# Kernel optimization log

Measured on AMD Instinct MI355X. Metric: run time of the kernel, lower is better.

## Reference

```python
import jax, jax.numpy as jnp
import numpy as np

H = 1536
NH = 24
HD = 64
B = 2
S = 2048


def _rotate_half(x):
    x1, x2 = x[..., : HD // 2], x[..., HD // 2 :]
    return jnp.concatenate((-x2, x1), axis=-1)


def setup_inputs() -> dict:
    key = jax.random.key(0)
    ks = jax.random.split(key, 8)
    scale = 1.0 / np.sqrt(H)
    pos = jnp.arange(S)[:, None]
    inv_freq = 1.0 / (10000.0 ** (jnp.arange(0, HD, 2, dtype=jnp.float32) / HD))
    ang = pos * inv_freq[None, :]
    ang = jnp.concatenate([ang, ang], axis=-1)  # [S, HD]
    return {
        "hidden_states": jax.random.normal(ks[0], (B, S, H), jnp.float32),
        "rope_cos": jnp.cos(ang),
        "rope_sin": jnp.sin(ang),
        "wq": jax.random.normal(ks[1], (H, H), jnp.float32) * scale,
        "bq": jnp.zeros((H,), jnp.float32),
        "wk": jax.random.normal(ks[2], (H, H), jnp.float32) * scale,
        "bk": jnp.zeros((H,), jnp.float32),
        "wv": jax.random.normal(ks[3], (H, H), jnp.float32) * scale,
        "bv": jnp.zeros((H,), jnp.float32),
        "wo": jax.random.normal(ks[4], (H, H), jnp.float32) * scale,
        "bo": jnp.zeros((H,), jnp.float32),
    }


def reference(hidden_states, rope_cos, rope_sin, wq, bq, wk, bk, wv, bv, wo, bo):
    b, s, _ = hidden_states.shape
    # QKV projections (torch Linear: x @ W.T + b)
    q = hidden_states @ wq.T + bq
    k = hidden_states @ wk.T + bk
    v = hidden_states @ wv.T + bv
    # [B, NH, S, HD]
    q = q.reshape(b, s, NH, HD).transpose(0, 2, 1, 3)
    k = k.reshape(b, s, NH, HD).transpose(0, 2, 1, 3)
    v = v.reshape(b, s, NH, HD).transpose(0, 2, 1, 3)
    # RoPE: cos/sin broadcast over batch & heads
    cos = rope_cos[None, None, :, :]
    sin = rope_sin[None, None, :, :]
    q = q * cos + _rotate_half(q) * sin
    k = k * cos + _rotate_half(k) * sin
    # SDPA
    scores = jnp.einsum("bhqd,bhkd->bhqk", q, k) / jnp.sqrt(jnp.float32(HD))
    attn = jax.nn.softmax(scores, axis=-1)
    out = jnp.einsum("bhqk,bhkd->bhqd", attn, v)
    out = out.transpose(0, 2, 1, 3).reshape(b, s, NH * HD)
    return out @ wo.T + bo
```

## Files before the change

kernel.cpp:

```cpp
#include <hip/hip_runtime.h>
#include <hip/hip_bf16.h>
#include <cstdint>

namespace {
constexpr int H_  = 1536;
constexpr int NH_ = 24;
constexpr int HD_ = 64;
constexpr int B_  = 2;
constexpr int S_  = 2048;
constexpr int M_  = B_ * S_;
constexpr int KD_ = H_;
}

typedef __attribute__((ext_vector_type(8)))  short bf16x8;
typedef __attribute__((ext_vector_type(4)))  float f32x4;
typedef __attribute__((ext_vector_type(16))) float f32x16;

__device__ __forceinline__ unsigned short f2bf_fast(float x) {
    return (unsigned short)((__float_as_uint(x) + 0x8000u) >> 16);
}
__device__ __forceinline__ unsigned pack2bf(float b_hi, float a_lo) {
    const unsigned ub = __float_as_uint(b_hi) + 0x8000u;
    const unsigned ua = __float_as_uint(a_lo) + 0x8000u;
    return (ub & 0xffff0000u) | (ua >> 16);
}

__device__ __forceinline__ void gload16(const short* g, short* l) {
    __builtin_amdgcn_global_load_lds(
        (const __attribute__((address_space(1))) unsigned int*)g,
        (__attribute__((address_space(3))) unsigned int*)l, 16, 0, 0);
}

__global__ __launch_bounds__(256)
void cast_all(const float* __restrict__ X,
              const float* __restrict__ wq, const float* __restrict__ wk,
              const float* __restrict__ wv, const float* __restrict__ wo,
              short* __restrict__ Xh,
              short* __restrict__ Wqh, short* __restrict__ Wkh,
              short* __restrict__ Wvh, short* __restrict__ Woh)
{
    constexpr int XB = (M_*H_) / 1024;
    constexpr int WB = (H_*H_) / 1024;
    const int bid = blockIdx.x;
    const float* src; short* dst; int off;
    if (bid < XB)            { src = X;  dst = Xh;  off = bid; }
    else {
        const int r = bid - XB, wsel = r / WB; off = r % WB;
        if      (wsel == 0)  { src = wq; dst = Wqh; }
        else if (wsel == 1)  { src = wk; dst = Wkh; }
        else if (wsel == 2)  { src = wv; dst = Wvh; }
        else                 { src = wo; dst = Woh; }
    }
    const int i = (off * 256 + threadIdx.x) * 4;
    const float4 v = *(const float4*)&src[i];
    uint2 o;
    o.x = pack2bf(v.y, v.x);
    o.y = pack2bf(v.w, v.z);
    *(uint2*)&dst[i] = o;
}

template<int KIND>
__global__ __launch_bounds__(256, 4)
void gemm_bf16(const short* __restrict__ A_g,
               const short* __restrict__ Wq, const short* __restrict__ Wk,
               const short* __restrict__ Wv,
               const float* __restrict__ bq, const float* __restrict__ bk,
               const float* __restrict__ bv,
               const float* __restrict__ cosb, const float* __restrict__ sinb,
               short* __restrict__ Qb, short* __restrict__ Kb,
               short* __restrict__ Vt, float* __restrict__ outf)
{
    __shared__ short Ah[128*64], Bh[128*64];

    const int t    = threadIdx.x;
    const int lane = t & 63;
    const int w    = t >> 6;
    const int wr   = w >> 1, wc = w & 1;
    const int l15  = lane & 15;
    const int grp  = lane >> 4;

    const int xcd = blockIdx.x & 7;
    const int off = blockIdx.x >> 3;
    const int m_idx = xcd * 4 + (off & 3);
    const int rest  = off >> 2;
    const int n_idx = rest % 12;
    const int zi    = (KIND == 0) ? rest / 12 : 3;

    const int m0 = m_idx * 128;
    const int n0 = n_idx * 128;

    const short* bhg; const float* bias;
    if (KIND == 0) {
        if      (zi == 0) { bhg = Wq; bias = bq; }
        else if (zi == 1) { bhg = Wk; bias = bk; }
        else              { bhg = Wv; bias = bv; }
    } else {
        bhg = Wq; bias = bq;
    }

    f32x4 acc[4][4];
#pragma unroll
    for (int i = 0; i < 4; ++i)
#pragma unroll
        for (int j = 0; j < 4; ++j) acc[i][j] = (f32x4){0.f, 0.f, 0.f, 0.f};

    const int srow  = lane >> 3;
    const int sslot = (lane & 7) ^ srow;

    for (int kt = 0; kt < KD_; kt += 64) {
        __syncthreads();
#pragma unroll
        for (int cc = 0; cc < 4; ++cc) {
            const int c = w * 4 + cc;
            const int r = c * 8 + srow;
            gload16(A_g + (size_t)(m0 + r) * KD_ + kt + sslot * 8, Ah + c * 512);
            gload16(bhg + (size_t)(n0 + r) * KD_ + kt + sslot * 8, Bh + c * 512);
        }
        __syncthreads();

#pragma unroll
        for (int kk = 0; kk < 2; ++kk) {
            bf16x8 af[4], bfr[4];
#pragma unroll
            for (int i = 0; i < 4; ++i) {
                const int ra = wr * 64 + i * 16 + l15;
                af[i]  = *(const bf16x8*)&Ah[ra * 64 + (((kk*4 + grp) ^ (ra & 7)) << 3)];
                const int rb = wc * 64 + i * 16 + l15;
                bfr[i] = *(const bf16x8*)&Bh[rb * 64 + (((kk*4 + grp) ^ (rb & 7)) << 3)];
            }
#pragma unroll
            for (int i = 0; i < 4; ++i)
#pragma unroll
                for (int j = 0; j < 4; ++j)
                    acc[i][j] = __builtin_amdgcn_mfma_f32_16x16x32_bf16(af[i], bfr[j], acc[i][j], 0, 0, 0);
        }
    }

    float bn[4];
#pragma unroll
    for (int ni = 0; ni < 4; ++ni) bn[ni] = bias[n0 + wc * 64 + ni * 16 + l15];
    const int hw = (n0 + wc * 64) >> 6;

    if (KIND == 1) {
#pragma unroll
        for (int mi = 0; mi < 4; ++mi)
#pragma unroll
            for (int r = 0; r < 4; ++r) {
                const int m = m0 + wr * 64 + mi * 16 + grp * 4 + r;
#pragma unroll
                for (int ni = 0; ni < 4; ++ni)
                    outf[(size_t)m * H_ + n0 + wc * 64 + ni * 16 + l15] =
                        acc[mi][ni][r] + bn[ni];
            }
        return;
    }

    if (zi == 2) {
        const int b = m0 >> 11;
#pragma unroll
        for (int mi = 0; mi < 4; ++mi) {
            const int sb = (m0 & (S_ - 1)) + wr * 64 + mi * 16 + grp * 4;
#pragma unroll
            for (int ni = 0; ni < 4; ++ni) {
                const int d = ni * 16 + l15;
                uint2 o;
                o.x = pack2bf(acc[mi][ni][1] + bn[ni], acc[mi][ni][0] + bn[ni]);
                o.y = pack2bf(acc[mi][ni][3] + bn[ni], acc[mi][ni][2] + bn[ni]);
                *(uint2*)&Vt[((size_t)(b * NH_ + hw) * HD_ + d) * S_ + sb] = o;
            }
        }
        return;
    }

    const float sc = (zi == 0) ? 0.18033688011112042f : 1.0f;
    short* dst = (zi == 0) ? Qb : Kb;
#pragma unroll
    for (int mi = 0; mi < 4; ++mi)
#pragma unroll
        for (int r = 0; r < 4; ++r) {
            const int m = m0 + wr * 64 + mi * 16 + grp * 4 + r;
            const int b = m >> 11;
            const int s = m & (S_ - 1);
#pragma unroll
            for (int ni = 0; ni < 4; ++ni) {
                const int d  = ni * 16 + l15;
                const float val = acc[mi][ni][r] + bn[ni];
                const float pv  = acc[mi][ni ^ 2][r] + bn[ni ^ 2];
                const float cs = cosb[s * HD_ + d];
                const float sn = sinb[s * HD_ + d];
                const float rot = (ni < 2) ? -pv : pv;
                dst[((size_t)(b * NH_ + hw) * S_ + s) * HD_ + d] =
                    (short)f2bf_fast((val * cs + rot * sn) * sc);
            }
        }
}

__global__ __launch_bounds__(256, 3)
void attn_mfma(const short* __restrict__ Q, const short* __restrict__ K,
               const short* __restrict__ Vt, short* __restrict__ AO)
{
    __shared__ short Ks[2][4096];
    __shared__ short Vs[2][4096];

    const int t    = threadIdx.x;
    const int lane = t & 63;
    const int wid  = t >> 6;
    const int bh   = blockIdx.y;
    const int q0   = blockIdx.x * 128;

    const int l31 = lane & 31;
    const int hi  = lane >> 5;
    const int sw7 = lane & 7;

    const short* Qg = Q  + ((size_t)bh * S_ + q0 + wid*32) * HD_;
    const short* Kg = K  + (size_t)bh * S_ * HD_;
    const short* Vg = Vt + (size_t)bh * HD_ * S_;

    bf16x8 qf[4];
#pragma unroll
    for (int kk = 0; kk < 4; ++kk)
        qf[kk] = *(const bf16x8*)(Qg + (size_t)l31*HD_ + kk*16 + hi*8);

    f32x16 oacc[2];
#pragma unroll
    for (int nt = 0; nt < 2; ++nt)
#pragma unroll
        for (int r = 0; r < 16; ++r) oacc[nt][r] = 0.f;
    float lacc = 0.f;

    auto stageKV = [&](int b, int kt) {
#pragma unroll
        for (int cc = 0; cc < 2; ++cc) {
            const int d   = cc * 256 + t;
            const int row = d >> 3;
            const int sg  = (d & 7) ^ (row & 7);
            gload16(Kg + (size_t)(kt + row) * HD_ + sg * 8, &Ks[b][d * 8]);
            gload16(Vg + (size_t)row * S_ + kt + sg * 8,    &Vs[b][d * 8]);
        }
    };

    stageKV(0, 0);
    __syncthreads();
    int cur = 0;

    for (int kt = 0; kt < S_; kt += 64) {
        if (kt + 64 < S_) stageKV(cur ^ 1, kt + 64);

        f32x16 sac[2];
#pragma unroll
        for (int nt = 0; nt < 2; ++nt)
#pragma unroll
            for (int r = 0; r < 16; ++r) sac[nt][r] = 0.f;
        __builtin_amdgcn_s_setprio(1);
#pragma unroll
        for (int kk = 0; kk < 4; ++kk) {
#pragma unroll
            for (int nt = 0; nt < 2; ++nt) {
                const int row = nt*32 + l31;
                const bf16x8 kfrag = *(const bf16x8*)
                    &Ks[cur][row*64 + (((kk*2 + hi) ^ sw7) << 3)];
                sac[nt] = __builtin_amdgcn_mfma_f32_32x32x16_bf16(kfrag, qf[kk], sac[nt], 0, 0, 0);
            }
        }
        __builtin_amdgcn_s_setprio(0);

#pragma unroll
        for (int nt = 0; nt < 2; ++nt)
#pragma unroll
            for (int r = 0; r < 16; ++r) {
                sac[nt][r] = exp2f(sac[nt][r]);
                lacc += sac[nt][r];
            }

        unsigned pw[4][4];
#pragma unroll
        for (int kk = 0; kk < 4; ++kk) {
            const int h  = kk >> 1;
            const int g2 = (kk & 1) * 2;
#pragma unroll
            for (int e = 0; e < 2; ++e) {
                unsigned A = pack2bf(sac[h][4*g2     + 2*e + 1], sac[h][4*g2     + 2*e]);
                unsigned Bv= pack2bf(sac[h][4*(g2+1) + 2*e + 1], sac[h][4*(g2+1) + 2*e]);
                asm volatile("v_permlane32_swap_b32 %0, %1" : "+v"(A), "+v"(Bv));
                pw[kk][e]     = A;
                pw[kk][e + 2] = Bv;
            }
        }

        __builtin_amdgcn_s_setprio(1);
#pragma unroll
        for (int ks = 0; ks < 4; ++ks) {
            union { unsigned u[4]; bf16x8 v; } pf;
            pf.u[0] = pw[ks][0]; pf.u[1] = pw[ks][1];
            pf.u[2] = pw[ks][2]; pf.u[3] = pw[ks][3];
#pragma unroll
            for (int nt = 0; nt < 2; ++nt) {
                const int row = nt*32 + l31;
                const bf16x8 vfrag = *(const bf16x8*)
                    &Vs[cur][row*64 + (((ks*2 + hi) ^ sw7) << 3)];
                oacc[nt] = __builtin_amdgcn_mfma_f32_32x32x16_bf16(vfrag, pf.v, oacc[nt], 0, 0, 0);
            }
        }
        __builtin_amdgcn_s_setprio(0);

        __syncthreads();
        cur ^= 1;
    }

    lacc += __shfl_xor(lacc, 32);
    const float inv = 1.f / lacc;

    const int b = bh / NH_, h = bh % NH_;
    const int srow = q0 + wid*32 + l31;
    const size_t rowb = ((size_t)(b*S_ + srow)) * H_ + h*HD_;
#pragma unroll
    for (int nt = 0; nt < 2; ++nt)
#pragma unroll
        for (int i = 0; i < 8; ++i) {
            const int crow = ((2*i) & 3) + 8*((2*i) >> 2) + 4*hi;
            const int d    = nt*32 + crow;
            *(unsigned*)&AO[rowb + d] =
                pack2bf(oacc[nt][2*i+1]*inv, oacc[nt][2*i]*inv);
        }
}

extern "C" void kernel_launch(void* const* d_in, const int* in_sizes, int n_in,
                              void* d_out, int out_size, void* d_ws, size_t ws_size,
                              hipStream_t stream)
{
    const float* X    = (const float*)d_in[0];
    const float* cosb = (const float*)d_in[1];
    const float* sinb = (const float*)d_in[2];
    const float* wq   = (const float*)d_in[3];
    const float* bq   = (const float*)d_in[4];
    const float* wk   = (const float*)d_in[5];
    const float* bk   = (const float*)d_in[6];
    const float* wv   = (const float*)d_in[7];
    const float* bv   = (const float*)d_in[8];
    const float* wo   = (const float*)d_in[9];
    const float* bo   = (const float*)d_in[10];
    float* out = (float*)d_out;

    const size_t MH = (size_t)M_ * H_;
    const size_t HH = (size_t)H_ * H_;

    short* Xh  = (short*)d_ws;
    short* Wqh = Xh  + MH;
    short* Wkh = Wqh + HH;
    short* Wvh = Wkh + HH;
    short* Woh = Wvh + HH;
    short* Qb  = Woh + HH;
    short* Kb  = Qb + MH;
    short* Vt  = Kb + MH;
    short* AO  = Vt + MH;

    cast_all<<<(int)(MH/1024 + 4*(HH/1024)), 256, 0, stream>>>(
        X, wq, wk, wv, wo, Xh, Wqh, Wkh, Wvh, Woh);

    gemm_bf16<0><<<1152, 256, 0, stream>>>(Xh, Wqh, Wkh, Wvh,
        bq, bk, bv, cosb, sinb, Qb, Kb, Vt, nullptr);

    attn_mfma<<<dim3(S_/128, B_*NH_), 256, 0, stream>>>(Qb, Kb, Vt, AO);

    gemm_bf16<1><<<384, 256, 0, stream>>>(AO, Woh, nullptr, nullptr,
        bo, nullptr, nullptr, nullptr, nullptr, nullptr, nullptr, nullptr, out);
}
```

Before: 217.8 us.

## Load attention K/V fragments directly from global memory, drop LDS staging

The attention kernel stops staging K and V tiles through double-buffered shared memory with barriers. Each wave now loads its MFMA K and V fragments straight from global memory into registers, relying on L2 reuse since all four waves read the same tiles. It also remaps the 1D grid so each XCD handles whole (batch, head) groups for cache locality, and uses the hardware exp2 builtin. This removes LDS traffic and the per-tile syncthreads, at the cost of four times the global/L2 load traffic, exposed load latency with no explicit prefetch, and higher register pressure now that the occupancy hint is gone.

```diff
diff --git a/kernel.cpp b/kernel.cpp
--- a/kernel.cpp
+++ b/kernel.cpp
@@ -23,6 +23,14 @@
     const unsigned ub = __float_as_uint(b_hi) + 0x8000u;
     const unsigned ua = __float_as_uint(a_lo) + 0x8000u;
     return (ub & 0xffff0000u) | (ua >> 16);
+}
+
+__device__ __forceinline__ float fast_exp2(float x) {
+#if __has_builtin(__builtin_amdgcn_exp2f)
+    return __builtin_amdgcn_exp2f(x);
+#else
+    return exp2f(x);
+#endif
 }
 
 __device__ __forceinline__ void gload16(const short* g, short* l) {
@@ -195,26 +203,28 @@
         }
 }
 
-__global__ __launch_bounds__(256, 3)
+__global__ __launch_bounds__(256)
 void attn_mfma(const short* __restrict__ Q, const short* __restrict__ K,
                const short* __restrict__ Vt, short* __restrict__ AO)
 {
-    __shared__ short Ks[2][4096];
-    __shared__ short Vs[2][4096];
-
     const int t    = threadIdx.x;
     const int lane = t & 63;
     const int wid  = t >> 6;
-    const int bh   = blockIdx.y;
-    const int q0   = blockIdx.x * 128;
+
+    const int bid = blockIdx.x;
+    const int xcd = bid & 7;
+    const int sq  = bid >> 3;
+    const int bh  = xcd * 6 + (sq >> 4);
+    const int q0  = (sq & 15) * 128;
 
     const int l31 = lane & 31;
     const int hi  = lane >> 5;
-    const int sw7 = lane & 7;
-
-    const short* Qg = Q  + ((size_t)bh * S_ + q0 + wid*32) * HD_;
-    const short* Kg = K  + (size_t)bh * S_ * HD_;
-    const short* Vg = Vt + (size_t)bh * HD_ * S_;
+
+    const short* Qg  = Q  + ((size_t)bh * S_ + q0 + wid*32) * HD_;
+    const short* Kg0 = K  + (size_t)bh * S_ * HD_ + l31*HD_ + hi*8;
+    const short* Kg1 = Kg0 + 32 * HD_;
+    const short* Vg0 = Vt + (size_t)bh * HD_ * S_ + (size_t)l31 * S_ + hi*8;
+    const short* Vg1 = Vg0 + (size_t)32 * S_;
 
     bf16x8 qf[4];
 #pragma unroll
@@ -228,23 +238,15 @@
         for (int r = 0; r < 16; ++r) oacc[nt][r] = 0.f;
     float lacc = 0.f;
 
-    auto stageKV = [&](int b, int kt) {
-#pragma unroll
-        for (int cc = 0; cc < 2; ++cc) {
-            const int d   = cc * 256 + t;
-            const int row = d >> 3;
-            const int sg  = (d & 7) ^ (row & 7);
-            gload16(Kg + (size_t)(kt + row) * HD_ + sg * 8, &Ks[b][d * 8]);
-            gload16(Vg + (size_t)row * S_ + kt + sg * 8,    &Vs[b][d * 8]);
-        }
-    };
-
-    stageKV(0, 0);
-    __syncthreads();
-    int cur = 0;
-
     for (int kt = 0; kt < S_; kt += 64) {
-        if (kt + 64 < S_) stageKV(cur ^ 1, kt + 64);
+        const short* kp0 = Kg0 + kt * HD_;
+        const short* kp1 = Kg1 + kt * HD_;
+        bf16x8 kf0[4], kf1[4];
+#pragma unroll
+        for (int kk = 0; kk < 4; ++kk) {
+            kf0[kk] = *(const bf16x8*)(kp0 + kk*16);
+            kf1[kk] = *(const bf16x8*)(kp1 + kk*16);
+        }
 
         f32x16 sac[2];
 #pragma unroll
@@ -254,21 +256,25 @@
         __builtin_amdgcn_s_setprio(1);
 #pragma unroll
         for (int kk = 0; kk < 4; ++kk) {
-#pragma unroll
-            for (int nt = 0; nt < 2; ++nt) {
-                const int row = nt*32 + l31;
-                const bf16x8 kfrag = *(const bf16x8*)
-                    &Ks[cur][row*64 + (((kk*2 + hi) ^ sw7) << 3)];
-                sac[nt] = __builtin_amdgcn_mfma_f32_32x32x16_bf16(kfrag, qf[kk], sac[nt], 0, 0, 0);
-            }
+            sac[0] = __builtin_amdgcn_mfma_f32_32x32x16_bf16(kf0[kk], qf[kk], sac[0], 0, 0, 0);
+            sac[1] = __builtin_amdgcn_mfma_f32_32x32x16_bf16(kf1[kk], qf[kk], sac[1], 0, 0, 0);
         }
         __builtin_amdgcn_s_setprio(0);
 
+        const short* vp0 = Vg0 + kt;
+        const short* vp1 = Vg1 + kt;
+        bf16x8 vf0[4], vf1[4];
+#pragma unroll
+        for (int ks = 0; ks < 4; ++ks) {
+            vf0[ks] = *(const bf16x8*)(vp0 + ks*16);
+            vf1[ks] = *(const bf16x8*)(vp1 + ks*16);
+        }
+
 #pragma unroll
         for (int nt = 0; nt < 2; ++nt)
 #pragma unroll
             for (int r = 0; r < 16; ++r) {
-                sac[nt][r] = exp2f(sac[nt][r]);
+                sac[nt][r] = fast_exp2(sac[nt][r]);
                 lacc += sac[nt][r];
             }
 
@@ -293,18 +299,10 @@
             union { unsigned u[4]; bf16x8 v; } pf;
             pf.u[0] = pw[ks][0]; pf.u[1] = pw[ks][1];
             pf.u[2] = pw[ks][2]; pf.u[3] = pw[ks][3];
-#pragma unroll
-            for (int nt = 0; nt < 2; ++nt) {
-                const int row = nt*32 + l31;
-                const bf16x8 vfrag = *(const bf16x8*)
-                    &Vs[cur][row*64 + (((ks*2 + hi) ^ sw7) << 3)];
-                oacc[nt] = __builtin_amdgcn_mfma_f32_32x32x16_bf16(vfrag, pf.v, oacc[nt], 0, 0, 0);
-            }
+            oacc[0] = __builtin_amdgcn_mfma_f32_32x32x16_bf16(vf0[ks], pf.v, oacc[0], 0, 0, 0);
+            oacc[1] = __builtin_amdgcn_mfma_f32_32x32x16_bf16(vf1[ks], pf.v, oacc[1], 0, 0, 0);
         }
         __builtin_amdgcn_s_setprio(0);
-
-        __syncthreads();
-        cur ^= 1;
     }
 
     lacc += __shfl_xor(lacc, 32);
@@ -360,7 +358,7 @@
     gemm_bf16<0><<<1152, 256, 0, stream>>>(Xh, Wqh, Wkh, Wvh,
         bq, bk, bv, cosb, sinb, Qb, Kb, Vt, nullptr);
 
-    attn_mfma<<<dim3(S_/128, B_*NH_), 256, 0, stream>>>(Qb, Kb, Vt, AO);
+    attn_mfma<<<768, 256, 0, stream>>>(Qb, Kb, Vt, AO);
 
     gemm_bf16<1><<<384, 256, 0, stream>>>(AO, Woh, nullptr, nullptr,
         bo, nullptr, nullptr, nullptr, nullptr, nullptr, nullptr, nullptr, out);
```

Result: slower. 293.6 us (+34.8%).
